# Kernel optimization log

Hardware: AMD Instinct MI355X
Metric: run time of the kernel (lower is better)

Reference implementation:

```python
import jax, jax.numpy as jnp
import numpy as np

N, E, C_IN, C_OUT, K, D_D = 50000, 800000, 16, 64, 3, 7


def setup_inputs() -> dict:
    key = jax.random.key(0)
    ks = jax.random.split(key, 10)
    s = 0.05
    x = jax.random.normal(ks[0], (N, C_IN), jnp.float32)
    edge_index = jax.random.randint(ks[1], (2, E), 0, N, dtype=jnp.int64)
    edge_weight = jax.random.uniform(ks[2], (E,), jnp.float32)
    h0 = jax.random.normal(ks[3], (N, C_OUT), jnp.float32)
    # stacked ChebConv params: gate order [z, r, h]
    Wx = jax.random.normal(ks[4], (3, K, C_IN, C_OUT), jnp.float32) * s
    Wh = jax.random.normal(ks[5], (3, K, C_OUT, C_OUT), jnp.float32) * s
    bx = jax.random.normal(ks[6], (3, C_OUT), jnp.float32) * s
    bh = jax.random.normal(ks[7], (3, C_OUT), jnp.float32) * s
    Wlin = jax.random.normal(ks[8], (C_OUT, D_D), jnp.float32) * s
    blin = jax.random.normal(ks[9], (D_D,), jnp.float32) * s
    return dict(x=x, edge_index=edge_index, edge_weight=edge_weight, h0=h0,
                Wx=Wx, Wh=Wh, bx=bx, bh=bh, Wlin=Wlin, blin=blin)


def _norm(src, dst, edge_weight, n):
    # ChebConv sym normalization with lambda_max=2:
    # L_sym = I - D^-1/2 A D^-1/2;  L_tilde = 2L/lambda_max - I = -D^-1/2 A D^-1/2
    w = jnp.where(src == dst, 0.0, edge_weight)  # remove self loops
    deg = jax.ops.segment_sum(w, src, num_segments=n)
    dinv = jnp.where(deg > 0, 1.0 / jnp.sqrt(deg), 0.0)
    return -dinv[src] * w * dinv[dst]


def _cheb(t, W, b, src, dst, nw, n):
    # K-hop Chebyshev recursion: Tx_{k+1} = 2*L~*Tx_k - Tx_{k-1}
    prop = lambda v: jax.ops.segment_sum(nw[:, None] * v[src], dst, num_segments=n)
    Tx0 = t
    out = Tx0 @ W[0]
    Tx1 = prop(Tx0)
    out = out + Tx1 @ W[1]
    for k in range(2, W.shape[0]):
        Tx2 = 2.0 * prop(Tx1) - Tx0
        out = out + Tx2 @ W[k]
        Tx0, Tx1 = Tx1, Tx2
    return out + b


def reference(x, edge_index, edge_weight, h0, Wx, Wh, bx, bh, Wlin, blin):
    n = x.shape[0]
    src, dst = edge_index[0], edge_index[1]
    nw = _norm(src, dst, edge_weight, n)
    z = jax.nn.sigmoid(_cheb(x, Wx[0], bx[0], src, dst, nw, n)
                       + _cheb(h0, Wh[0], bh[0], src, dst, nw, n))
    r = jax.nn.sigmoid(_cheb(x, Wx[1], bx[1], src, dst, nw, n)
                       + _cheb(h0, Wh[1], bh[1], src, dst, nw, n))
    htil = jnp.tanh(_cheb(x, Wx[2], bx[2], src, dst, nw, n)
                    + _cheb(h0 * r, Wh[2], bh[2], src, dst, nw, n))
    h = z * h0 + (1.0 - z) * htil
    y = jax.nn.relu(h) @ Wlin + blin
    return (jax.lax.stop_gradient(h), y)
```

## Files before the change

### kernel.cpp

```cpp
#include <hip/hip_runtime.h>

constexpr int NN = 50000;
constexpr int NE = 800000;
constexpr int CI = 16;
constexpr int CO = 64;
constexpr int DD = 7;

typedef __bf16 bf16x8 __attribute__((ext_vector_type(8)));
typedef float  f32x4  __attribute__((ext_vector_type(4)));
typedef float  f32x2  __attribute__((ext_vector_type(2)));

__device__ inline float blo(unsigned u) { return __uint_as_float(u << 16); }
__device__ inline float bhi(unsigned u) { return __uint_as_float(u & 0xffff0000u); }

__device__ inline void acc8_fp8(float acc[8], float w, uint2 u) {
    f32x2 c;
    c = __builtin_amdgcn_cvt_pk_f32_fp8(u.x, false); acc[0] += w * c[0]; acc[1] += w * c[1];
    c = __builtin_amdgcn_cvt_pk_f32_fp8(u.x, true);  acc[2] += w * c[0]; acc[3] += w * c[1];
    c = __builtin_amdgcn_cvt_pk_f32_fp8(u.y, false); acc[4] += w * c[0]; acc[5] += w * c[1];
    c = __builtin_amdgcn_cvt_pk_f32_fp8(u.y, true);  acc[6] += w * c[0]; acc[7] += w * c[1];
}
__device__ inline uint2 pack_fp8x8(const float o[8]) {
    int t0 = __builtin_amdgcn_cvt_pk_fp8_f32(o[0], o[1], 0, false);
    t0 = __builtin_amdgcn_cvt_pk_fp8_f32(o[2], o[3], t0, true);
    int t1 = __builtin_amdgcn_cvt_pk_fp8_f32(o[4], o[5], 0, false);
    t1 = __builtin_amdgcn_cvt_pk_fp8_f32(o[6], o[7], t1, true);
    uint2 r; r.x = (unsigned)t0; r.y = (unsigned)t1; return r;
}
__device__ inline unsigned char fp8_of(float v) {
    return (unsigned char)(__builtin_amdgcn_cvt_pk_fp8_f32(v, v, 0, false) & 0xff);
}


constexpr int EB = (NE + 255) / 256;
constexpr int XOCT = NN * CI / 8;
constexpr int HOCT = NN * CO / 8;
constexpr int CB = (XOCT + HOCT + 255) / 256;

__global__ void __launch_bounds__(256) k_deg_cast_prep(
    const int* __restrict__ src, const int* __restrict__ dst, const float* __restrict__ ew,
    float* __restrict__ deg, int* __restrict__ count, unsigned short* __restrict__ rank,
    const float* __restrict__ x, const float* __restrict__ h0,
    __bf16* __restrict__ x_bf, __bf16* __restrict__ h0_bf, unsigned char* __restrict__ h0_f8,
    const float* __restrict__ Wx, const float* __restrict__ Wh,
    const float* __restrict__ bx, const float* __restrict__ bh,
    bf16x8* __restrict__ BfragZR, bf16x8* __restrict__ BfragHT, float* __restrict__ biasC) {
    int b = blockIdx.x;
    if (b < EB) {
        int e = b * 256 + threadIdx.x;
        if (e >= NE) return;
        int s = src[e], d = dst[e];
        float w = (s == d) ? 0.f : ew[e];
        atomicAdd(&deg[s], w);
        rank[e] = (unsigned short)atomicAdd(&count[d], 1);
    } else if (b < EB + CB) {
        int t = (b - EB) * 256 + threadIdx.x;
        if (t < XOCT) {
            const float* sp = x + (size_t)t * 8;
            float4 a = *(const float4*)sp;
            float4 c = *(const float4*)(sp + 4);
            bf16x8 o;
            o[0] = (__bf16)a.x; o[1] = (__bf16)a.y; o[2] = (__bf16)a.z; o[3] = (__bf16)a.w;
            o[4] = (__bf16)c.x; o[5] = (__bf16)c.y; o[6] = (__bf16)c.z; o[7] = (__bf16)c.w;
            *(bf16x8*)(x_bf + (size_t)t * 8) = o;
        } else if (t < XOCT + HOCT) {
            int u = t - XOCT;
            const float* sp = h0 + (size_t)u * 8;
            float4 a = *(const float4*)sp;
            float4 c = *(const float4*)(sp + 4);
            bf16x8 o;
            o[0] = (__bf16)a.x; o[1] = (__bf16)a.y; o[2] = (__bf16)a.z; o[3] = (__bf16)a.w;
            o[4] = (__bf16)c.x; o[5] = (__bf16)c.y; o[6] = (__bf16)c.z; o[7] = (__bf16)c.w;
            *(bf16x8*)(h0_bf + (size_t)u * 8) = o;
            float f[8] = {a.x, a.y, a.z, a.w, c.x, c.y, c.z, c.w};
            *(uint2*)(h0_f8 + (size_t)u * 8) = pack_fp8x8(f);
        }
    } else {
        int tid = (b - EB - CB) * 256 + threadIdx.x;
        if (tid < 6144) {
            int e = tid, gate, n, kk, l;
            if (e < 4096) {
                int t = e >> 9, rem = e & 511;
                kk = rem >> 6; l = rem & 63;
                n = t * 16 + (l & 15);
                gate = n >> 6;
            } else {
                int e2 = e - 4096;
                int t = e2 >> 9, rem = e2 & 511;
                kk = rem >> 6; l = rem & 63;
                n = t * 16 + (l & 15);
                gate = 2;
            }
            int co = n & 63;
            int k0 = kk * 32 + (l >> 4) * 8;
            bf16x8 f;
#pragma unroll
            for (int j = 0; j < 8; j++) {
                int k = k0 + j;
                float w = 0.f;
                if (k < 48) {
                    int kb = k >> 4, ci = k & 15;
                    const float* Wg = Wx + gate * 3 * 16 * 64;
                    float w0 = Wg[(kb * 16 + ci) * 64 + co];
                    if (kb == 0)      w = w0 - Wg[(2 * 16 + ci) * 64 + co];
                    else if (kb == 1) w = w0;
                    else              w = 2.f * w0;
                } else if (k < 240) {
                    int kh = k - 48, kb = kh >> 6, ci = kh & 63;
                    const float* Wg = Wh + gate * 3 * 64 * 64;
                    float w0 = Wg[(kb * 64 + ci) * 64 + co];
                    if (kb == 0)      w = w0 - Wg[(2 * 64 + ci) * 64 + co];
                    else if (kb == 1) w = w0;
                    else              w = 2.f * w0;
                }
                f[j] = (__bf16)w;
            }
            if (e < 4096) BfragZR[e] = f; else BfragHT[e - 4096] = f;
        } else if (tid < 6144 + 192) {
            int i = tid - 6144;
            biasC[i] = bx[i] + bh[i];
        }
    }
}


__global__ void k_scan1(const int* __restrict__ count, int* __restrict__ S, int* __restrict__ bsums) {
    __shared__ int ts[256];
    int tid = threadIdx.x;
    int base = blockIdx.x * 1024;
    int vals[4]; int s = 0;
#pragma unroll
    for (int j = 0; j < 4; j++) {
        int idx = base + tid * 4 + j;
        int v = (idx < NN) ? count[idx] : 0;
        s += v; vals[j] = s;
    }
    ts[tid] = s;
    __syncthreads();
    for (int off = 1; off < 256; off <<= 1) {
        int v = (tid >= off) ? ts[tid - off] : 0;
        __syncthreads();
        ts[tid] += v;
        __syncthreads();
    }
    int prev = (tid > 0) ? ts[tid - 1] : 0;
#pragma unroll
    for (int j = 0; j < 4; j++) {
        int idx = base + tid * 4 + j;
        if (idx < NN) S[idx] = vals[j] + prev;
    }
    if (tid == 255) bsums[blockIdx.x] = ts[255];
}

__global__ void k_scan23(const int* __restrict__ S, const int* __restrict__ bsums,
                         int* __restrict__ rowptr, float* __restrict__ deg) {
    int i = blockIdx.x * 256 + threadIdx.x;
    if (i >= NN) return;
    int chunk = blockIdx.x >> 2;
    int pre = 0;
    for (int j = 0; j < chunk; j++) pre += bsums[j];
    int tot = S[i] + pre;
    rowptr[i + 1] = tot;
    if (i == 0) rowptr[0] = 0;
    float d = deg[i];
    deg[i] = (d > 0.f) ? (1.f / sqrtf(d)) : 0.f;
}

__global__ void k_place(const int* __restrict__ src, const int* __restrict__ dst,
                        const float* __restrict__ ew, const unsigned short* __restrict__ rank,
                        const float* __restrict__ dinv, const int* __restrict__ rowptr,
                        unsigned* __restrict__ csr_ew) {
    int e = blockIdx.x * 256 + threadIdx.x;
    if (e >= NE) return;
    int s = src[e], d = dst[e];
    float w = (s == d) ? 0.f : ew[e];
    float wp = dinv[s] * w;
    __bf16 wb = (__bf16)wp;
    unsigned short ub = __builtin_bit_cast(unsigned short, wb);
    csr_ew[rowptr[d] + rank[e]] = (unsigned)s | ((unsigned)ub << 16);
}


__device__ inline void prop64_body(int n, int lane,
                                   const unsigned char* __restrict__ v8,
                                   const float* __restrict__ dinv,
                                   const int* __restrict__ rowptr,
                                   const unsigned* __restrict__ ew,
                                   __bf16* __restrict__ out_bf,
                                   unsigned char* __restrict__ out_f8) {
    int j = lane >> 3, cg = lane & 7;
    int beg = rowptr[n], end = rowptr[n + 1];
    float acc[8] = {0.f, 0.f, 0.f, 0.f, 0.f, 0.f, 0.f, 0.f};
    for (int e = beg + j; e < end; e += 8) {
        unsigned p = ew[e];
        float w = bhi(p);
        int s = p & 0xffff;
        uint2 u = *(const uint2*)(v8 + (size_t)s * 64 + cg * 8);
        acc8_fp8(acc, w, u);
    }
#pragma unroll
    for (int m = 8; m <= 32; m <<= 1) {
#pragma unroll
        for (int i = 0; i < 8; i++) acc[i] += __shfl_xor(acc[i], m, 64);
    }
    if (lane < 8) {
        float f = -dinv[n];
        float o[8];
#pragma unroll
        for (int i = 0; i < 8; i++) o[i] = f * acc[i];
        bf16x8 st;
#pragma unroll
        for (int i = 0; i < 8; i++) st[i] = (__bf16)o[i];
        *(bf16x8*)(out_bf + (size_t)n * 64 + lane * 8) = st;
        if (out_f8) *(uint2*)(out_f8 + (size_t)n * 64 + lane * 8) = pack_fp8x8(o);
    }
}

__device__ inline void prop16_body(int n, int lane,
                                   const __bf16* __restrict__ v,
                                   const float* __restrict__ dinv,
                                   const int* __restrict__ rowptr,
                                   const unsigned* __restrict__ ew, __bf16* __restrict__ out) {
    int j = lane >> 1, cg = lane & 1;
    int beg = rowptr[n], end = rowptr[n + 1];
    float acc[8] = {0.f, 0.f, 0.f, 0.f, 0.f, 0.f, 0.f, 0.f};
    for (int e = beg + j; e < end; e += 32) {
        unsigned p = ew[e];
        float w = bhi(p);
        int s = p & 0xffff;
        uint4 u = *(const uint4*)((const char*)v + ((size_t)s * 32 + cg * 16));
        acc[0] += w * blo(u.x); acc[1] += w * bhi(u.x);
        acc[2] += w * blo(u.y); acc[3] += w * bhi(u.y);
        acc[4] += w * blo(u.z); acc[5] += w * bhi(u.z);
        acc[6] += w * blo(u.w); acc[7] += w * bhi(u.w);
    }
#pragma unroll
    for (int m = 2; m <= 32; m <<= 1) {
#pragma unroll
        for (int i = 0; i < 8; i++) acc[i] += __shfl_xor(acc[i], m, 64);
    }
    if (lane < 2) {
        float f = -dinv[n];
        bf16x8 st;
#pragma unroll
        for (int i = 0; i < 8; i++) st[i] = (__bf16)(f * acc[i]);
        *(bf16x8*)(out + (size_t)n * 16 + lane * 8) = st;
    }
}

__global__ void __launch_bounds__(256) k_stage(
    const unsigned char* __restrict__ vh8, const __bf16* __restrict__ vx,
    const float* __restrict__ dinv,
    const int* __restrict__ rowptr, const unsigned* __restrict__ ew,
    __bf16* __restrict__ outh_bf, unsigned char* __restrict__ outh_f8,
    __bf16* __restrict__ outx) {
    int gw = blockIdx.x * 4 + (threadIdx.x >> 6);
    int lane = threadIdx.x & 63;
    if (gw < NN) prop64_body(gw, lane, vh8, dinv, rowptr, ew, outh_bf, outh_f8);
    else if (gw < 2 * NN) prop16_body(gw - NN, lane, vx, dinv, rowptr, ew, outx);
}

__global__ void __launch_bounds__(256) k_prop64(
    const unsigned char* __restrict__ v8, const float* __restrict__ dinv,
    const int* __restrict__ rowptr, const unsigned* __restrict__ ew,
    __bf16* __restrict__ out_bf, unsigned char* __restrict__ out_f8) {
    int n = blockIdx.x * 4 + (threadIdx.x >> 6);
    if (n >= NN) return;
    prop64_body(n, threadIdx.x & 63, v8, dinv, rowptr, ew, out_bf, out_f8);
}


__device__ inline bf16x8 load_a_bf(int c, int m,
                                   const __bf16* __restrict__ xb, const __bf16* __restrict__ t1,
                                   const __bf16* __restrict__ t2, const __bf16* __restrict__ hb,
                                   const __bf16* __restrict__ h1, const __bf16* __restrict__ h2) {
    if (c >= 30) {
        bf16x8 a;
#pragma unroll
        for (int j = 0; j < 8; j++) a[j] = (__bf16)0.f;
        return a;
    }
    if (c < 6) {
        const __bf16* base = (c < 2) ? xb : ((c < 4) ? t1 : t2);
        return *(const bf16x8*)(base + (size_t)m * 16 + (c & 1) * 8);
    }
    int d = c - 6;
    const __bf16* base = (d < 8) ? hb : ((d < 16) ? h1 : h2);
    return *(const bf16x8*)(base + (size_t)m * 64 + (d & 7) * 8);
}

__global__ void __launch_bounds__(256) k_mfma_zr(
    const __bf16* __restrict__ xb, const __bf16* __restrict__ t1, const __bf16* __restrict__ t2,
    const __bf16* __restrict__ hb, const __bf16* __restrict__ h1, const __bf16* __restrict__ h2,
    const bf16x8* __restrict__ Bfrag, const float* __restrict__ biasC,
    __bf16* __restrict__ z_bf, __bf16* __restrict__ hr_bf, unsigned char* __restrict__ hr_f8) {
    int wv = (blockIdx.x * 256 + threadIdx.x) >> 6;
    if (wv >= NN / 16) return;
    int lane = threadIdx.x & 63;
    int q = lane >> 4, r16 = lane & 15;
    int ma = wv * 16 + r16;
    f32x4 acc[8];
#pragma unroll
    for (int t = 0; t < 8; t++) acc[t] = (f32x4){0.f, 0.f, 0.f, 0.f};
#pragma unroll
    for (int kk = 0; kk < 8; kk++) {
        bf16x8 a = load_a_bf(kk * 4 + q, ma, xb, t1, t2, hb, h1, h2);
#pragma unroll
        for (int t = 0; t < 8; t++)
            acc[t] = __builtin_amdgcn_mfma_f32_16x16x32_bf16(a, Bfrag[(t * 8 + kk) * 64 + lane], acc[t], 0, 0, 0);
    }
    int mbase = wv * 16 + q * 4;
#pragma unroll
    for (int t = 0; t < 8; t++) {
        int co = t * 16 + r16;
        float bias = biasC[co];
        int col = co & 63;
#pragma unroll
        for (int reg = 0; reg < 4; reg++) {
            int mm = mbase + reg;
            float p = acc[t][reg] + bias;
            float s = 1.f / (1.f + __expf(-p));
            if (t < 4) z_bf[(size_t)mm * 64 + col] = (__bf16)s;
            else {
                float hrv = s * (float)hb[(size_t)mm * 64 + col];
                hr_bf[(size_t)mm * 64 + col] = (__bf16)hrv;
                hr_f8[(size_t)mm * 64 + col] = fp8_of(hrv);
            }
        }
    }
}

__global__ void __launch_bounds__(256) k_mfma_ht(
    const __bf16* __restrict__ xb, const __bf16* __restrict__ t1, const __bf16* __restrict__ t2,
    const __bf16* __restrict__ hrb, const __bf16* __restrict__ r1, const __bf16* __restrict__ r2,
    const bf16x8* __restrict__ Bfrag, const float* __restrict__ biasC,
    const __bf16* __restrict__ z_bf, const float* __restrict__ h0,
    const float* __restrict__ Wlin, const float* __restrict__ blin,
    float* __restrict__ hout, float* __restrict__ yout) {
    int wv = (blockIdx.x * 256 + threadIdx.x) >> 6;
    if (wv >= NN / 16) return;
    int lane = threadIdx.x & 63;
    int q = lane >> 4, r16 = lane & 15;
    int ma = wv * 16 + r16;
    f32x4 acc[4];
#pragma unroll
    for (int t = 0; t < 4; t++) acc[t] = (f32x4){0.f, 0.f, 0.f, 0.f};
#pragma unroll
    for (int kk = 0; kk < 8; kk++) {
        bf16x8 a = load_a_bf(kk * 4 + q, ma, xb, t1, t2, hrb, r1, r2);
#pragma unroll
        for (int t = 0; t < 4; t++)
            acc[t] = __builtin_amdgcn_mfma_f32_16x16x32_bf16(a, Bfrag[(t * 8 + kk) * 64 + lane], acc[t], 0, 0, 0);
    }
    int mbase = wv * 16 + q * 4;
    float hbuf[4][4];
#pragma unroll
    for (int t = 0; t < 4; t++) {
        int co = t * 16 + r16;
        float bias = biasC[128 + co];
#pragma unroll
        for (int reg = 0; reg < 4; reg++) {
            int mm = mbase + reg;
            float p = acc[t][reg] + bias;
            float htl = tanhf(p);
            float zv = (float)z_bf[(size_t)mm * 64 + co];
            float h0v = h0[(size_t)mm * 64 + co];
            float hn = zv * h0v + (1.f - zv) * htl;
            hout[(size_t)mm * 64 + co] = hn;
            hbuf[t][reg] = hn;
        }
    }
    float ya[4][DD];
#pragma unroll
    for (int reg = 0; reg < 4; reg++)
#pragma unroll
        for (int d = 0; d < DD; d++) ya[reg][d] = 0.f;
#pragma unroll
    for (int t = 0; t < 4; t++) {
        int cb = (t * 16 + r16) * DD;
        float wl[DD];
#pragma unroll
        for (int d = 0; d < DD; d++) wl[d] = Wlin[cb + d];
#pragma unroll
        for (int reg = 0; reg < 4; reg++) {
            float rh = fmaxf(hbuf[t][reg], 0.f);
#pragma unroll
            for (int d = 0; d < DD; d++) ya[reg][d] += rh * wl[d];
        }
    }
#pragma unroll
    for (int m = 1; m <= 8; m <<= 1) {
#pragma unroll
        for (int reg = 0; reg < 4; reg++)
#pragma unroll
            for (int d = 0; d < DD; d++) ya[reg][d] += __shfl_xor(ya[reg][d], m, 64);
    }
    if (r16 < DD) {
        float b = blin[r16];
#pragma unroll
        for (int reg = 0; reg < 4; reg++) {
            float v = (r16 == 0) ? ya[reg][0] : (r16 == 1) ? ya[reg][1] : (r16 == 2) ? ya[reg][2]
                    : (r16 == 3) ? ya[reg][3] : (r16 == 4) ? ya[reg][4] : (r16 == 5) ? ya[reg][5]
                    : ya[reg][6];
            yout[(size_t)(mbase + reg) * DD + r16] = v + b;
        }
    }
}


extern "C" void kernel_launch(void* const* d_in, const int* in_sizes, int n_in,
                              void* d_out, int out_size, void* d_ws, size_t ws_size,
                              hipStream_t stream) {
    (void)in_sizes; (void)n_in; (void)out_size; (void)ws_size;
    const float* x    = (const float*)d_in[0];
    const int*   eidx = (const int*)d_in[1];
    const float* ew   = (const float*)d_in[2];
    const float* h0   = (const float*)d_in[3];
    const float* Wx   = (const float*)d_in[4];
    const float* Wh   = (const float*)d_in[5];
    const float* bx   = (const float*)d_in[6];
    const float* bh   = (const float*)d_in[7];
    const float* Wlin = (const float*)d_in[8];
    const float* blin = (const float*)d_in[9];
    const int* src = eidx;
    const int* dst = eidx + NE;

    char* ws = (char*)d_ws;
    size_t off = 0;
    auto alloc = [&](size_t nbytes) -> void* {
        void* p = ws + off;
        off += (nbytes + 255) & ~(size_t)255;
        return p;
    };
    float*  dinv    = (float*)alloc(NN * 4);
    int*    count   = (int*)alloc(NN * 4);
    int*    S       = (int*)alloc(NN * 4);
    int*    rowptr  = (int*)alloc((NN + 1) * 4);
    int*    bsums   = (int*)alloc(64 * 4);
    unsigned short* rank = (unsigned short*)alloc((size_t)NE * 2);
    unsigned* csr_ew = (unsigned*)alloc((size_t)NE * 4);
    __bf16* x_bf    = (__bf16*)alloc((size_t)NN * CI * 2);
    __bf16* h0_bf   = (__bf16*)alloc((size_t)NN * CO * 2);
    unsigned char* h0_f8 = (unsigned char*)alloc((size_t)NN * CO);
    unsigned char* T1_f8 = (unsigned char*)alloc((size_t)NN * CO);
    unsigned char* hr_f8 = (unsigned char*)alloc((size_t)NN * CO);
    __bf16* Tx1     = (__bf16*)alloc((size_t)NN * CI * 2);
    __bf16* Tx2     = (__bf16*)alloc((size_t)NN * CI * 2);
    __bf16* Th1     = (__bf16*)alloc((size_t)NN * CO * 2);
    __bf16* Th2     = (__bf16*)alloc((size_t)NN * CO * 2);
    __bf16* hr_bf   = (__bf16*)alloc((size_t)NN * CO * 2);
    __bf16* z_bf    = (__bf16*)alloc((size_t)NN * CO * 2);
    bf16x8* BfragZR = (bf16x8*)alloc(4096 * 16);
    bf16x8* BfragHT = (bf16x8*)alloc(2048 * 16);
    float*  biasC   = (float*)alloc(192 * 4);

    float* hout = (float*)d_out;
    float* yout = hout + (size_t)NN * CO;

    constexpr int NB = (NN + 1023) / 1024;
    const int NBLK = (NN + 255) / 256;
    const int PROPB = (NN + 3) / 4;
    const int STAGEB = (2 * NN + 3) / 4;
    const int GEMMB = (NN / 16 * 64 + 255) / 256;

    hipMemsetAsync(dinv, 0, NN * 4, stream);
    hipMemsetAsync(count, 0, NN * 4, stream);

    k_deg_cast_prep<<<EB + CB + 25, 256, 0, stream>>>(
        src, dst, ew, dinv, count, rank, x, h0, x_bf, h0_bf, h0_f8,
        Wx, Wh, bx, bh, BfragZR, BfragHT, biasC);
    k_scan1<<<NB, 256, 0, stream>>>(count, S, bsums);
    k_scan23<<<NBLK, 256, 0, stream>>>(S, bsums, rowptr, dinv);
    k_place<<<EB, 256, 0, stream>>>(src, dst, ew, rank, dinv, rowptr, csr_ew);

    k_stage<<<STAGEB, 256, 0, stream>>>(h0_f8, x_bf, dinv, rowptr, csr_ew, Th1, T1_f8, Tx1);
    k_stage<<<STAGEB, 256, 0, stream>>>(T1_f8, Tx1, dinv, rowptr, csr_ew, Th2, nullptr, Tx2);

    k_mfma_zr<<<GEMMB, 256, 0, stream>>>(x_bf, Tx1, Tx2, h0_bf, Th1, Th2,
                                         BfragZR, biasC, z_bf, hr_bf, hr_f8);
    k_prop64<<<PROPB, 256, 0, stream>>>(hr_f8, dinv, rowptr, csr_ew, Th1, T1_f8);
    k_prop64<<<PROPB, 256, 0, stream>>>(T1_f8, dinv, rowptr, csr_ew, Th2, nullptr);
    k_mfma_ht<<<GEMMB, 256, 0, stream>>>(x_bf, Tx1, Tx2, hr_bf, Th1, Th2,
                                         BfragHT, biasC, z_bf, h0, Wlin, blin, hout, yout);
}
```

Baseline: 363.6 us.

## Privatize degree and count atomics per XCD with workgroup-scope atomics

Replaces the global degree and in-degree atomics with per-XCD private copies (indexed by the hardware XCC id) updated with relaxed workgroup-scope atomics, so the atomics stay in each die's L2 instead of going device-wide. The scan kernels then sum the eight copies and compute per-XCD offsets inside each CSR row. The edge kernel also writes a packed 8-byte edge record (src, dst, rank, xcd, bf16 weight) so k_place no longer re-reads src, dst and ew. The risks are correctness: workgroup scope does not make the atomics coherent across workgroups on one XCD, the packing assumes node ids fit in 16 bits (NN=50000 does) and per-XCD ranks below 256, and the bf16-rounded weight now feeds the normalization. The cost is eight times the memset and scan traffic.

```diff
diff --git a/kernel.cpp b/kernel.cpp
--- a/kernel.cpp
+++ b/kernel.cpp
@@ -5,6 +5,7 @@
 constexpr int CI = 16;
 constexpr int CO = 64;
 constexpr int DD = 7;
+constexpr int NXCD = 8;
 
 typedef __bf16 bf16x8 __attribute__((ext_vector_type(8)));
 typedef float  f32x4  __attribute__((ext_vector_type(4)));
@@ -12,6 +13,18 @@
 
 __device__ inline float blo(unsigned u) { return __uint_as_float(u << 16); }
 __device__ inline float bhi(unsigned u) { return __uint_as_float(u & 0xffff0000u); }
+
+__device__ inline unsigned xcc_id() {
+    unsigned v;
+    asm volatile("s_getreg_b32 %0, hwreg(HW_REG_XCC_ID)" : "=s"(v));
+    return v & 7;
+}
+__device__ inline int l2_add_ret(int* p, int v) {
+    return __hip_atomic_fetch_add(p, v, __ATOMIC_RELAXED, __HIP_MEMORY_SCOPE_WORKGROUP);
+}
+__device__ inline void l2_add_f(float* p, float v) {
+    __hip_atomic_fetch_add(p, v, __ATOMIC_RELAXED, __HIP_MEMORY_SCOPE_WORKGROUP);
+}
 
 __device__ inline void acc8_fp8(float acc[8], float w, uint2 u) {
     f32x2 c;
@@ -39,7 +52,7 @@
 
 __global__ void __launch_bounds__(256) k_deg_cast_prep(
     const int* __restrict__ src, const int* __restrict__ dst, const float* __restrict__ ew,
-    float* __restrict__ deg, int* __restrict__ count, unsigned short* __restrict__ rank,
+    float* __restrict__ deg8, int* __restrict__ count8, uint2* __restrict__ erec,
     const float* __restrict__ x, const float* __restrict__ h0,
     __bf16* __restrict__ x_bf, __bf16* __restrict__ h0_bf, unsigned char* __restrict__ h0_f8,
     const float* __restrict__ Wx, const float* __restrict__ Wh,
@@ -51,8 +64,13 @@
         if (e >= NE) return;
         int s = src[e], d = dst[e];
         float w = (s == d) ? 0.f : ew[e];
-        atomicAdd(&deg[s], w);
-        rank[e] = (unsigned short)atomicAdd(&count[d], 1);
+        unsigned xc = xcc_id();
+        l2_add_f(&deg8[xc * NN + s], w);
+        int rk = l2_add_ret(&count8[xc * NN + d], 1);
+        __bf16 wb = (__bf16)w;
+        unsigned wu = (unsigned)__builtin_bit_cast(unsigned short, wb);
+        erec[e] = make_uint2((unsigned)s | ((unsigned)d << 16),
+                             ((unsigned)rk & 0xff) | (xc << 8) | (wu << 16));
     } else if (b < EB + CB) {
         int t = (b - EB) * 256 + threadIdx.x;
         if (t < XOCT) {
@@ -124,7 +142,7 @@
 }
 
 
-__global__ void k_scan1(const int* __restrict__ count, int* __restrict__ S, int* __restrict__ bsums) {
+__global__ void k_scan1(const int* __restrict__ count8, int* __restrict__ S, int* __restrict__ bsums) {
     __shared__ int ts[256];
     int tid = threadIdx.x;
     int base = blockIdx.x * 1024;
@@ -132,7 +150,11 @@
 #pragma unroll
     for (int j = 0; j < 4; j++) {
         int idx = base + tid * 4 + j;
-        int v = (idx < NN) ? count[idx] : 0;
+        int v = 0;
+        if (idx < NN) {
+#pragma unroll
+            for (int xc = 0; xc < NXCD; xc++) v += count8[xc * NN + idx];
+        }
         s += v; vals[j] = s;
     }
     ts[tid] = s;
@@ -153,7 +175,9 @@
 }
 
 __global__ void k_scan23(const int* __restrict__ S, const int* __restrict__ bsums,
-                         int* __restrict__ rowptr, float* __restrict__ deg) {
+                         const int* __restrict__ count8, const float* __restrict__ deg8,
+                         int* __restrict__ rowptr, int* __restrict__ off8,
+                         float* __restrict__ dinv) {
     int i = blockIdx.x * 256 + threadIdx.x;
     if (i >= NN) return;
     int chunk = blockIdx.x >> 2;
@@ -162,22 +186,30 @@
     int tot = S[i] + pre;
     rowptr[i + 1] = tot;
     if (i == 0) rowptr[0] = 0;
-    float d = deg[i];
-    deg[i] = (d > 0.f) ? (1.f / sqrtf(d)) : 0.f;
-}
-
-__global__ void k_place(const int* __restrict__ src, const int* __restrict__ dst,
-                        const float* __restrict__ ew, const unsigned short* __restrict__ rank,
-                        const float* __restrict__ dinv, const int* __restrict__ rowptr,
-                        unsigned* __restrict__ csr_ew) {
+    int c[NXCD]; int ctot = 0;
+#pragma unroll
+    for (int xc = 0; xc < NXCD; xc++) { c[xc] = count8[xc * NN + i]; ctot += c[xc]; }
+    int run = tot - ctot;
+#pragma unroll
+    for (int xc = 0; xc < NXCD; xc++) { off8[xc * NN + i] = run; run += c[xc]; }
+    float dsum = 0.f;
+#pragma unroll
+    for (int xc = 0; xc < NXCD; xc++) dsum += deg8[xc * NN + i];
+    dinv[i] = (dsum > 0.f) ? (1.f / sqrtf(dsum)) : 0.f;
+}
+
+__global__ void k_place(const uint2* __restrict__ erec, const float* __restrict__ dinv,
+                        const int* __restrict__ off8, unsigned* __restrict__ csr_ew) {
     int e = blockIdx.x * 256 + threadIdx.x;
     if (e >= NE) return;
-    int s = src[e], d = dst[e];
-    float w = (s == d) ? 0.f : ew[e];
+    uint2 r = erec[e];
+    int s = r.x & 0xffff, d = r.x >> 16;
+    unsigned rk = r.y & 0xff, xc = (r.y >> 8) & 7;
+    float w = bhi(r.y);
     float wp = dinv[s] * w;
     __bf16 wb = (__bf16)wp;
     unsigned short ub = __builtin_bit_cast(unsigned short, wb);
-    csr_ew[rowptr[d] + rank[e]] = (unsigned)s | ((unsigned)ub << 16);
+    csr_ew[off8[xc * NN + d] + rk] = (unsigned)s | ((unsigned)ub << 16);
 }
 
 
@@ -432,12 +464,14 @@
         off += (nbytes + 255) & ~(size_t)255;
         return p;
     };
+    float*  deg8    = (float*)alloc((size_t)NXCD * NN * 4);
+    int*    count8  = (int*)alloc((size_t)NXCD * NN * 4);
+    int*    off8    = (int*)alloc((size_t)NXCD * NN * 4);
     float*  dinv    = (float*)alloc(NN * 4);
-    int*    count   = (int*)alloc(NN * 4);
     int*    S       = (int*)alloc(NN * 4);
     int*    rowptr  = (int*)alloc((NN + 1) * 4);
     int*    bsums   = (int*)alloc(64 * 4);
-    unsigned short* rank = (unsigned short*)alloc((size_t)NE * 2);
+    uint2*  erec    = (uint2*)alloc((size_t)NE * 8);
     unsigned* csr_ew = (unsigned*)alloc((size_t)NE * 4);
     __bf16* x_bf    = (__bf16*)alloc((size_t)NN * CI * 2);
     __bf16* h0_bf   = (__bf16*)alloc((size_t)NN * CO * 2);
@@ -463,15 +497,15 @@
     const int STAGEB = (2 * NN + 3) / 4;
     const int GEMMB = (NN / 16 * 64 + 255) / 256;
 
-    hipMemsetAsync(dinv, 0, NN * 4, stream);
-    hipMemsetAsync(count, 0, NN * 4, stream);
+    hipMemsetAsync(deg8, 0, (size_t)NXCD * NN * 4, stream);
+    hipMemsetAsync(count8, 0, (size_t)NXCD * NN * 4, stream);
 
     k_deg_cast_prep<<<EB + CB + 25, 256, 0, stream>>>(
-        src, dst, ew, dinv, count, rank, x, h0, x_bf, h0_bf, h0_f8,
+        src, dst, ew, deg8, count8, erec, x, h0, x_bf, h0_bf, h0_f8,
         Wx, Wh, bx, bh, BfragZR, BfragHT, biasC);
-    k_scan1<<<NB, 256, 0, stream>>>(count, S, bsums);
-    k_scan23<<<NBLK, 256, 0, stream>>>(S, bsums, rowptr, dinv);
-    k_place<<<EB, 256, 0, stream>>>(src, dst, ew, rank, dinv, rowptr, csr_ew);
+    k_scan1<<<NB, 256, 0, stream>>>(count8, S, bsums);
+    k_scan23<<<NBLK, 256, 0, stream>>>(S, bsums, count8, deg8, rowptr, off8, dinv);
+    k_place<<<EB, 256, 0, stream>>>(erec, dinv, off8, csr_ew);
 
     k_stage<<<STAGEB, 256, 0, stream>>>(h0_f8, x_bf, dinv, rowptr, csr_ew, Th1, T1_f8, Tx1);
     k_stage<<<STAGEB, 256, 0, stream>>>(T1_f8, Tx1, dinv, rowptr, csr_ew, Th2, nullptr, Tx2);
```

New measurement: 359.3 us. About the same (-1.2%).
